# Kernel optimization log

Hardware: AMD Instinct MI355X
Metric: run time of the kernel (lower is better)

Reference implementation:

```python
import jax, jax.numpy as jnp
import numpy as np

B, N, D_MODEL, H, D_K, D_V = 2, 2048, 1024, 16, 64, 64


def setup_inputs() -> dict:
    key = jax.random.key(0)
    ks = jax.random.split(key, 8)
    queries = jax.random.normal(ks[0], (B, N, D_MODEL), dtype=jnp.float32)
    keys = jax.random.normal(ks[1], (B, N, D_MODEL), dtype=jnp.float32)
    values = jax.random.normal(ks[2], (B, N, D_MODEL), dtype=jnp.float32)
    # nn.Linear weights: (out_features, in_features); init.normal_(std=0.001) in the
    # original, but we use a larger scale for a numerically meaningful test.
    Wq = jax.random.normal(ks[3], (H * D_K, D_MODEL), dtype=jnp.float32) * 0.02
    Wk = jax.random.normal(ks[4], (H * D_K, D_MODEL), dtype=jnp.float32) * 0.02
    Wv = jax.random.normal(ks[5], (H * D_V, D_MODEL), dtype=jnp.float32) * 0.02
    Wo = jax.random.normal(ks[6], (D_MODEL, H * D_V), dtype=jnp.float32) * 0.02
    bo = jnp.zeros((D_MODEL,), dtype=jnp.float32)
    return {"queries": queries, "keys": keys, "values": values,
            "Wq": Wq, "Wk": Wk, "Wv": Wv, "Wo": Wo, "bo": bo}


def reference(queries, keys, values, Wq, Wk, Wv, Wo, bo):
    b, nq, _ = queries.shape
    nk = keys.shape[1]
    scale = 1.0 / np.sqrt(D_K).astype(np.float32)
    # projections: (b, n, h, d)
    q = (queries @ Wq.T).reshape(b, nq, H, D_K)
    k = (keys @ Wk.T).reshape(b, nk, H, D_K)
    v = (values @ Wv.T).reshape(b, nk, H, D_V)
    # scaled dot-product attention; seq_mask=None, attention_weights=None, dropout p=0
    att = jnp.einsum('bqhd,bkhd->bhqk', q, k) * scale  # (b, h, nq, nk)
    att = jax.nn.softmax(att, axis=-1)
    out = jnp.einsum('bhqk,bkhd->bqhd', att, v).reshape(b, nq, H * D_V)
    return queries + (out @ Wo.T + bo)
```

## Files before the change

### kernel.cpp

```cpp
#include <hip/hip_runtime.h>
#include <hip/hip_bf16.h>
#include <stdint.h>

#define BATCH  2
#define SEQ    2048
#define DMODEL 1024
#define NHEAD  16
#define DHEAD  64

typedef unsigned short u16;
typedef __attribute__((ext_vector_type(8))) short bf16x8;
typedef __attribute__((ext_vector_type(4))) float f32x4;

__device__ __forceinline__ u16 f2bf(float x) {
    union { float f; uint32_t u; } v; v.f = x;
    uint32_t r = v.u + 0x7fffu + ((v.u >> 16) & 1u);
    return (u16)(r >> 16);
}

__device__ __forceinline__ uint32_t pk2bf(float a, float b) {
    __hip_bfloat162 h = __float22bfloat162_rn(make_float2(a, b));
    return *(uint32_t*)&h;
}

__device__ __forceinline__ float exp2_raw(float x) {
    float r;
    asm("v_exp_f32 %0, %1" : "=v"(r) : "v"(x));
    return r;
}

__device__ __forceinline__ void gload_lds16(const void* g, void* l) {
    __builtin_amdgcn_global_load_lds(
        (const __attribute__((address_space(1))) uint32_t*)(uintptr_t)g,
        (__attribute__((address_space(3))) uint32_t*)(uintptr_t)l,
        16, 0, 0);
}

__device__ __forceinline__ f32x4 mfma16(bf16x8 a, bf16x8 b, f32x4 c) {
    return __builtin_amdgcn_mfma_f32_16x16x32_bf16(a, b, c, 0, 0, 0);
}

__global__ __launch_bounds__(256) void cvt7_kernel(
    const float* s0, const float* s1, const float* s2, const float* s3,
    const float* s4, const float* s5, const float* s6,
    u16* d0, u16* d1, u16* d2, u16* d3, u16* d4, u16* d5, u16* d6)
{
    const float* s; u16* d; size_t n;
    switch (blockIdx.y) {
        case 0: s = s0; d = d0; n = (size_t)BATCH * SEQ * DMODEL; break;
        case 1: s = s1; d = d1; n = (size_t)BATCH * SEQ * DMODEL; break;
        case 2: s = s2; d = d2; n = (size_t)BATCH * SEQ * DMODEL; break;
        case 3: s = s3; d = d3; n = (size_t)DMODEL * DMODEL; break;
        case 4: s = s4; d = d4; n = (size_t)DMODEL * DMODEL; break;
        case 5: s = s5; d = d5; n = (size_t)DMODEL * DMODEL; break;
        default: s = s6; d = d6; n = (size_t)DMODEL * DMODEL; break;
    }
    size_t i = ((size_t)blockIdx.x * 256 + threadIdx.x) * 8;
    if (i >= n) return;
    float4 a = *(const float4*)(s + i);
    float4 b = *(const float4*)(s + i + 4);
    union { uint4 v; u16 e[8]; } u;
    u.e[0] = f2bf(a.x); u.e[1] = f2bf(a.y); u.e[2] = f2bf(a.z); u.e[3] = f2bf(a.w);
    u.e[4] = f2bf(b.x); u.e[5] = f2bf(b.y); u.e[6] = f2bf(b.z); u.e[7] = f2bf(b.w);
    *(uint4*)(d + i) = u.v;
}

__device__ __forceinline__ void gemm_core_128(
    const u16* __restrict__ A, const u16* __restrict__ Bm, int K,
    int brow, int bcol, u16* As, u16* Bs, f32x4 (&acc)[4][4])
{
    const int tid  = threadIdx.x;
    const int lane = tid & 63;
    const int wr   = ((tid >> 6) >> 1) * 64;
    const int wc   = ((tid >> 6) & 1) * 64;
    const int srow = tid >> 2;
    const int scol = (tid & 3) * 8;
    const int fr   = lane & 15;
    const int fk   = (lane >> 4) * 8;

    for (int k0 = 0; k0 < K; k0 += 32) {
        gload_lds16(A  + (size_t)(brow + srow) * K + k0 + scol,       As + srow * 32 + scol);
        gload_lds16(A  + (size_t)(brow + 64 + srow) * K + k0 + scol,  As + (64 + srow) * 32 + scol);
        gload_lds16(Bm + (size_t)(bcol + srow) * K + k0 + scol,       Bs + srow * 32 + scol);
        gload_lds16(Bm + (size_t)(bcol + 64 + srow) * K + k0 + scol,  Bs + (64 + srow) * 32 + scol);
        __syncthreads();
        bf16x8 af[4], bfv[4];
        #pragma unroll
        for (int i = 0; i < 4; ++i) {
            af[i]  = *(const bf16x8*)(As + (wr + i * 16 + fr) * 32 + fk);
            bfv[i] = *(const bf16x8*)(Bs + (wc + i * 16 + fr) * 32 + fk);
        }
        #pragma unroll
        for (int am = 0; am < 4; ++am)
            #pragma unroll
            for (int bn = 0; bn < 4; ++bn)
                acc[am][bn] = mfma16(af[am], bfv[bn], acc[am][bn]);
        __syncthreads();
    }
}

__device__ __forceinline__ void gemm_core_64x128(
    const u16* __restrict__ A, const u16* __restrict__ Bm, int K,
    int brow, int bcol, u16* As, u16* Bs, f32x4 (&acc)[4][2])
{
    const int tid  = threadIdx.x;
    const int lane = tid & 63;
    const int wc   = (tid >> 6) * 32;
    const int srow = tid >> 2;
    const int scol = (tid & 3) * 8;
    const int fr   = lane & 15;
    const int fk   = (lane >> 4) * 8;

    for (int k0 = 0; k0 < K; k0 += 32) {
        gload_lds16(A  + (size_t)(brow + srow) * K + k0 + scol,       As + srow * 32 + scol);
        gload_lds16(Bm + (size_t)(bcol + srow) * K + k0 + scol,       Bs + srow * 32 + scol);
        gload_lds16(Bm + (size_t)(bcol + 64 + srow) * K + k0 + scol,  Bs + (64 + srow) * 32 + scol);
        __syncthreads();
        bf16x8 af[4], bfv[2];
        #pragma unroll
        for (int i = 0; i < 4; ++i)
            af[i]  = *(const bf16x8*)(As + (i * 16 + fr) * 32 + fk);
        #pragma unroll
        for (int i = 0; i < 2; ++i)
            bfv[i] = *(const bf16x8*)(Bs + (wc + i * 16 + fr) * 32 + fk);
        #pragma unroll
        for (int am = 0; am < 4; ++am)
            #pragma unroll
            for (int bn = 0; bn < 2; ++bn)
                acc[am][bn] = mfma16(af[am], bfv[bn], acc[am][bn]);
        __syncthreads();
    }
}

__global__ __launch_bounds__(256) void gemm_qkv_kernel(
    const u16* __restrict__ Xq, const u16* __restrict__ Xk, const u16* __restrict__ Xv,
    const u16* __restrict__ Wq, const u16* __restrict__ Wk, const u16* __restrict__ Wv,
    u16* __restrict__ Qo, u16* __restrict__ Ko, u16* __restrict__ Vt,
    int M, int Nn, int K)
{
    __shared__ u16 As[128 * 32];
    __shared__ u16 Bs[128 * 32];
    const int z = blockIdx.z;
    const u16* A  = (z == 0) ? Xq : (z == 1) ? Xk : Xv;
    const u16* Bm = (z == 0) ? Wq : (z == 1) ? Wk : Wv;
    const float scale = (z == 0) ? 0.18033688011112042f : 1.0f;

    const int lin  = blockIdx.y * gridDim.x + blockIdx.x;
    const int nlin = (lin & 7) * 32 + (lin >> 3);
    const int brow = (nlin >> 3) * 128;
    const int bcol = (nlin & 7) * 128;
    f32x4 acc[4][4];
    #pragma unroll
    for (int am = 0; am < 4; ++am)
        #pragma unroll
        for (int bn = 0; bn < 4; ++bn)
            acc[am][bn] = (f32x4){0.f, 0.f, 0.f, 0.f};

    gemm_core_128(A, Bm, K, brow, bcol, As, Bs, acc);

    const int lane = threadIdx.x & 63;
    const int wr = ((threadIdx.x >> 6) >> 1) * 64;
    const int wc = ((threadIdx.x >> 6) & 1) * 64;
    const int fr = lane & 15;
    const int fj4 = (lane >> 4) * 4;

    if (z == 2) {
        #pragma unroll
        for (int am = 0; am < 4; ++am)
            #pragma unroll
            for (int bn = 0; bn < 4; ++bn) {
                int row = brow + wr + am * 16 + fj4;
                int col = bcol + wc + bn * 16 + fr;
                int b   = row >> 11;
                int n   = row & 2047;
                int h   = col >> 6;
                int d   = col & 63;
                uint2 w;
                w.x = pk2bf(acc[am][bn][0], acc[am][bn][1]);
                w.y = pk2bf(acc[am][bn][2], acc[am][bn][3]);
                *(uint2*)(Vt + ((size_t)(b * 16 + h) * DHEAD + d) * SEQ + n) = w;
            }
    } else {
        u16* D = (z == 0) ? Qo : Ko;
        #pragma unroll
        for (int am = 0; am < 4; ++am)
            #pragma unroll
            for (int bn = 0; bn < 4; ++bn)
                #pragma unroll
                for (int j = 0; j < 4; ++j) {
                    int row = brow + wr + am * 16 + fj4 + j;
                    int col = bcol + wc + bn * 16 + fr;
                    D[(size_t)row * Nn + col] = f2bf(acc[am][bn][j] * scale);
                }
    }
}

__global__ __launch_bounds__(256, 2) void gemm_out_kernel(
    const u16* __restrict__ A, const u16* __restrict__ Bm,
    const float* __restrict__ bias, const float* __restrict__ resid,
    float* __restrict__ D, int M, int Nn, int K)
{
    __shared__ u16 As[64 * 32];
    __shared__ u16 Bs[128 * 32];

    const int lin  = blockIdx.y * gridDim.x + blockIdx.x;
    const int nlin = (lin & 7) * 64 + (lin >> 3);
    const int brow = (nlin >> 3) * 64;
    const int bcol = (nlin & 7) * 128;
    f32x4 acc[4][2];
    #pragma unroll
    for (int am = 0; am < 4; ++am)
        #pragma unroll
        for (int bn = 0; bn < 2; ++bn)
            acc[am][bn] = (f32x4){0.f, 0.f, 0.f, 0.f};

    gemm_core_64x128(A, Bm, K, brow, bcol, As, Bs, acc);

    const int lane = threadIdx.x & 63;
    const int wc = (threadIdx.x >> 6) * 32;
    const int fr = lane & 15;
    const int fj4 = (lane >> 4) * 4;
    #pragma unroll
    for (int am = 0; am < 4; ++am)
        #pragma unroll
        for (int bn = 0; bn < 2; ++bn)
            #pragma unroll
            for (int j = 0; j < 4; ++j) {
                int row = brow + am * 16 + fj4 + j;
                int col = bcol + wc + bn * 16 + fr;
                D[(size_t)row * Nn + col] = acc[am][bn][j] + bias[col] + resid[(size_t)row * Nn + col];
            }
}

__global__ __launch_bounds__(1024, 1) void attn_kernel(
    const u16* __restrict__ Qb, const u16* __restrict__ Kb, const u16* __restrict__ Vt,
    u16* __restrict__ AO)
{
    __shared__ u16 Ks[3][64 * 64];
    __shared__ u16 Vs[3][64 * 64];
    __shared__ u16 Ps[256 * 72];

    const int tid  = threadIdx.x;
    const int lane = tid & 63;
    const int wave = tid >> 6;

    const int lin  = blockIdx.x;
    const int nlin = (lin & 7) * 32 + (lin >> 3);
    const int qblk = nlin & 7;
    const int bh   = nlin >> 3;

    const size_t rowbase = (size_t)(bh >> 4) * SEQ;
    const int colbase = (bh & 15) * DHEAD;
    const int q0 = qblk * 256;
    const int fr  = lane & 15;
    const int g   = lane >> 4;
    const int fk  = g * 8;
    const int fj4 = g * 4;
    const int qw  = wave * 16;

    const u16* Kh = Kb + rowbase * DMODEL + colbase;
    const u16* Vh = Vt + (size_t)bh * DHEAD * SEQ;

    const int st  = tid & 511;
    const int sr  = st >> 3;
    const int sc  = st & 7;
    const int scs = (sc ^ (sr & 7)) << 3;
    const int sdst = sr * 64 + sc * 8;
    const bool stageK = (tid < 512);

    bf16x8 qf[2];
    #pragma unroll
    for (int kc = 0; kc < 2; ++kc)
        qf[kc] = *(const bf16x8*)(Qb + (rowbase + q0 + qw + fr) * DMODEL
                                     + colbase + kc * 32 + fk);

    f32x4 oacc[4];
    float lsum = 0.f;
    #pragma unroll
    for (int dn = 0; dn < 4; ++dn) oacc[dn] = (f32x4){0.f, 0.f, 0.f, 0.f};

    if (stageK) {
        gload_lds16(Kh + (size_t)sr * DMODEL + scs,        &Ks[0][sdst]);
        gload_lds16(Kh + (size_t)(64 + sr) * DMODEL + scs, &Ks[1][sdst]);
    } else {
        gload_lds16(Vh + (size_t)sr * SEQ + scs,           &Vs[0][sdst]);
        gload_lds16(Vh + (size_t)sr * SEQ + 64 + scs,      &Vs[1][sdst]);
    }

    const int NT = SEQ / 64;
    int cur = 0;
    for (int t = 0; t < NT; ++t) {
        if (t < NT - 1) {
            asm volatile("s_waitcnt vmcnt(1)" ::: "memory");
        } else {
            asm volatile("s_waitcnt vmcnt(0)" ::: "memory");
        }
        __builtin_amdgcn_s_barrier();
        __builtin_amdgcn_sched_barrier(0);

        if (t + 2 < NT) {
            int wbuf = cur + 2; if (wbuf >= 3) wbuf -= 3;
            const size_t kvn = (size_t)(t + 2) * 64;
            if (stageK) gload_lds16(Kh + (kvn + sr) * DMODEL + scs,    &Ks[wbuf][sdst]);
            else        gload_lds16(Vh + (size_t)sr * SEQ + kvn + scs, &Vs[wbuf][sdst]);
        }

        const u16* K0 = &Ks[cur][0];
        const u16* V0 = &Vs[cur][0];

        f32x4 sacc[4];
        #pragma unroll
        for (int bn = 0; bn < 4; ++bn) sacc[bn] = (f32x4){0.f, 0.f, 0.f, 0.f};
        __builtin_amdgcn_s_setprio(1);
        #pragma unroll
        for (int bn = 0; bn < 4; ++bn) {
            bf16x8 kf0 = *(const bf16x8*)(K0 + (bn * 16 + fr) * 64 + (((g)     ^ (fr & 7)) << 3));
            bf16x8 kf1 = *(const bf16x8*)(K0 + (bn * 16 + fr) * 64 + (((4 + g) ^ (fr & 7)) << 3));
            sacc[bn] = mfma16(kf0, qf[0], sacc[bn]);
            sacc[bn] = mfma16(kf1, qf[1], sacc[bn]);
        }
        __builtin_amdgcn_s_setprio(0);

        {
            float lacc = 0.f;
            #pragma unroll
            for (int bn = 0; bn < 4; ++bn) {
                float p0 = exp2_raw(sacc[bn][0]);
                float p1 = exp2_raw(sacc[bn][1]);
                float p2 = exp2_raw(sacc[bn][2]);
                float p3 = exp2_raw(sacc[bn][3]);
                uint2 w;
                w.x = pk2bf(p0, p1);
                w.y = pk2bf(p2, p3);
                *(uint2*)(Ps + (qw + fr) * 72 + bn * 16 + fj4) = w;
                lacc += (p0 + p1) + (p2 + p3);
            }
            lsum += lacc;
        }

        bf16x8 pf[2];
        #pragma unroll
        for (int kc = 0; kc < 2; ++kc)
            pf[kc] = *(const bf16x8*)(Ps + (qw + fr) * 72 + kc * 32 + fk);
        __builtin_amdgcn_s_setprio(1);
        #pragma unroll
        for (int dn = 0; dn < 4; ++dn) {
            bf16x8 vf0 = *(const bf16x8*)(V0 + (dn * 16 + fr) * 64 + (((g)     ^ (fr & 7)) << 3));
            bf16x8 vf1 = *(const bf16x8*)(V0 + (dn * 16 + fr) * 64 + (((4 + g) ^ (fr & 7)) << 3));
            oacc[dn] = mfma16(pf[0], vf0, oacc[dn]);
            oacc[dn] = mfma16(pf[1], vf1, oacc[dn]);
        }
        __builtin_amdgcn_s_setprio(0);

        cur = (cur == 2) ? 0 : cur + 1;
    }

    float invj[4];
    {
        float l = lsum;
        l += __shfl_xor(l, 16);
        l += __shfl_xor(l, 32);
        #pragma unroll
        for (int j = 0; j < 4; ++j) {
            float lj = __shfl(l, (lane & 48) | (fj4 + j));
            invj[j] = 1.f / lj;
        }
    }

    #pragma unroll
    for (int dn = 0; dn < 4; ++dn)
        #pragma unroll
        for (int j = 0; j < 4; ++j) {
            int row = q0 + qw + fj4 + j;
            AO[(rowbase + row) * DMODEL + colbase + dn * 16 + fr] =
                f2bf(oacc[dn][j] * invj[j]);
        }
}

extern "C" void kernel_launch(void* const* d_in, const int* in_sizes, int n_in,
                              void* d_out, int out_size, void* d_ws, size_t ws_size,
                              hipStream_t stream)
{
    const float* q_f  = (const float*)d_in[0];
    const float* k_f  = (const float*)d_in[1];
    const float* v_f  = (const float*)d_in[2];
    const float* Wq_f = (const float*)d_in[3];
    const float* Wk_f = (const float*)d_in[4];
    const float* Wv_f = (const float*)d_in[5];
    const float* Wo_f = (const float*)d_in[6];
    const float* bo_f = (const float*)d_in[7];

    char* ws = (char*)d_ws;
    const size_t ACT = (size_t)BATCH * SEQ * DMODEL * sizeof(u16);
    const size_t WSZ = (size_t)DMODEL * DMODEL * sizeof(u16);
    u16* Xq  = (u16*)(ws);
    u16* Xk  = (u16*)(ws + ACT);
    u16* Xv  = (u16*)(ws + 2 * ACT);
    u16* Wqb = (u16*)(ws + 3 * ACT);
    u16* Wkb = (u16*)(ws + 3 * ACT + WSZ);
    u16* Wvb = (u16*)(ws + 3 * ACT + 2 * WSZ);
    u16* Wob = (u16*)(ws + 3 * ACT + 3 * WSZ);
    u16* Qb  = (u16*)(ws + 3 * ACT + 4 * WSZ);
    u16* Kb  = (u16*)(ws + 4 * ACT + 4 * WSZ);
    u16* Vt  = (u16*)(ws + 5 * ACT + 4 * WSZ);
    u16* AO  = (u16*)(ws + 6 * ACT + 4 * WSZ);

    const int M = BATCH * SEQ;
    const int Nn = DMODEL;
    const int K = DMODEL;

    cvt7_kernel<<<dim3(2048, 7, 1), 256, 0, stream>>>(
        q_f, k_f, v_f, Wq_f, Wk_f, Wv_f, Wo_f,
        Xq, Xk, Xv, Wqb, Wkb, Wvb, Wob);

    gemm_qkv_kernel<<<dim3(Nn / 128, M / 128, 3), 256, 0, stream>>>(
        Xq, Xk, Xv, Wqb, Wkb, Wvb, Qb, Kb, Vt, M, Nn, K);

    attn_kernel<<<dim3(256, 1, 1), 1024, 0, stream>>>(Qb, Kb, Vt, AO);

    gemm_out_kernel<<<dim3(Nn / 128, M / 64, 1), 256, 0, stream>>>(
        AO, Wob, bo_f, q_f, (float*)d_out, M, Nn, K);
}
```

Before: 123.4 us.

## Fuse fp32-to-bf16 activation conversion into QKV GEMM A-tile loads

The standalone conversion pass over the three fp32 activation tensors is removed. The QKV GEMM now reads the fp32 activations directly, converts them to bf16 in registers and stores them into LDS, while the weights are still pre-converted by a smaller kernel. This avoids writing and re-reading roughly 24 MB of bf16 activation copies. In exchange the A loads now go through registers instead of the async global-to-LDS path, each tile re-reads fp32 data at twice the byte width, and every column tile repeats the conversion.

```diff
diff --git a/kernel.cpp b/kernel.cpp
--- a/kernel.cpp
+++ b/kernel.cpp
@@ -40,23 +40,18 @@
     return __builtin_amdgcn_mfma_f32_16x16x32_bf16(a, b, c, 0, 0, 0);
 }
 
-__global__ __launch_bounds__(256) void cvt7_kernel(
+__global__ __launch_bounds__(256) void cvt4_kernel(
     const float* s0, const float* s1, const float* s2, const float* s3,
-    const float* s4, const float* s5, const float* s6,
-    u16* d0, u16* d1, u16* d2, u16* d3, u16* d4, u16* d5, u16* d6)
-{
-    const float* s; u16* d; size_t n;
+    u16* d0, u16* d1, u16* d2, u16* d3)
+{
+    const float* s; u16* d;
     switch (blockIdx.y) {
-        case 0: s = s0; d = d0; n = (size_t)BATCH * SEQ * DMODEL; break;
-        case 1: s = s1; d = d1; n = (size_t)BATCH * SEQ * DMODEL; break;
-        case 2: s = s2; d = d2; n = (size_t)BATCH * SEQ * DMODEL; break;
-        case 3: s = s3; d = d3; n = (size_t)DMODEL * DMODEL; break;
-        case 4: s = s4; d = d4; n = (size_t)DMODEL * DMODEL; break;
-        case 5: s = s5; d = d5; n = (size_t)DMODEL * DMODEL; break;
-        default: s = s6; d = d6; n = (size_t)DMODEL * DMODEL; break;
+        case 0: s = s0; d = d0; break;
+        case 1: s = s1; d = d1; break;
+        case 2: s = s2; d = d2; break;
+        default: s = s3; d = d3; break;
     }
     size_t i = ((size_t)blockIdx.x * 256 + threadIdx.x) * 8;
-    if (i >= n) return;
     float4 a = *(const float4*)(s + i);
     float4 b = *(const float4*)(s + i + 4);
     union { uint4 v; u16 e[8]; } u;
@@ -65,8 +60,8 @@
     *(uint4*)(d + i) = u.v;
 }
 
-__device__ __forceinline__ void gemm_core_128(
-    const u16* __restrict__ A, const u16* __restrict__ Bm, int K,
+__device__ __forceinline__ void gemm_core_128_f32A(
+    const float* __restrict__ A, const u16* __restrict__ Bm, int K,
     int brow, int bcol, u16* As, u16* Bs, f32x4 (&acc)[4][4])
 {
     const int tid  = threadIdx.x;
@@ -79,8 +74,21 @@
     const int fk   = (lane >> 4) * 8;
 
     for (int k0 = 0; k0 < K; k0 += 32) {
-        gload_lds16(A  + (size_t)(brow + srow) * K + k0 + scol,       As + srow * 32 + scol);
-        gload_lds16(A  + (size_t)(brow + 64 + srow) * K + k0 + scol,  As + (64 + srow) * 32 + scol);
+        {
+            const float* s0 = A + (size_t)(brow + srow) * K + k0 + scol;
+            const float* s1 = A + (size_t)(brow + 64 + srow) * K + k0 + scol;
+            float4 a0 = *(const float4*)(s0);
+            float4 a1 = *(const float4*)(s0 + 4);
+            float4 b0 = *(const float4*)(s1);
+            float4 b1 = *(const float4*)(s1 + 4);
+            uint4 wA, wB;
+            wA.x = pk2bf(a0.x, a0.y); wA.y = pk2bf(a0.z, a0.w);
+            wA.z = pk2bf(a1.x, a1.y); wA.w = pk2bf(a1.z, a1.w);
+            wB.x = pk2bf(b0.x, b0.y); wB.y = pk2bf(b0.z, b0.w);
+            wB.z = pk2bf(b1.x, b1.y); wB.w = pk2bf(b1.z, b1.w);
+            *(uint4*)(As + srow * 32 + scol) = wA;
+            *(uint4*)(As + (64 + srow) * 32 + scol) = wB;
+        }
         gload_lds16(Bm + (size_t)(bcol + srow) * K + k0 + scol,       Bs + srow * 32 + scol);
         gload_lds16(Bm + (size_t)(bcol + 64 + srow) * K + k0 + scol,  Bs + (64 + srow) * 32 + scol);
         __syncthreads();
@@ -133,7 +141,7 @@
 }
 
 __global__ __launch_bounds__(256) void gemm_qkv_kernel(
-    const u16* __restrict__ Xq, const u16* __restrict__ Xk, const u16* __restrict__ Xv,
+    const float* __restrict__ Xq, const float* __restrict__ Xk, const float* __restrict__ Xv,
     const u16* __restrict__ Wq, const u16* __restrict__ Wk, const u16* __restrict__ Wv,
     u16* __restrict__ Qo, u16* __restrict__ Ko, u16* __restrict__ Vt,
     int M, int Nn, int K)
@@ -141,8 +149,8 @@
     __shared__ u16 As[128 * 32];
     __shared__ u16 Bs[128 * 32];
     const int z = blockIdx.z;
-    const u16* A  = (z == 0) ? Xq : (z == 1) ? Xk : Xv;
-    const u16* Bm = (z == 0) ? Wq : (z == 1) ? Wk : Wv;
+    const float* A = (z == 0) ? Xq : (z == 1) ? Xk : Xv;
+    const u16* Bm  = (z == 0) ? Wq : (z == 1) ? Wk : Wv;
     const float scale = (z == 0) ? 0.18033688011112042f : 1.0f;
 
     const int lin  = blockIdx.y * gridDim.x + blockIdx.x;
@@ -156,7 +164,7 @@
         for (int bn = 0; bn < 4; ++bn)
             acc[am][bn] = (f32x4){0.f, 0.f, 0.f, 0.f};
 
-    gemm_core_128(A, Bm, K, brow, bcol, As, Bs, acc);
+    gemm_core_128_f32A(A, Bm, K, brow, bcol, As, Bs, acc);
 
     const int lane = threadIdx.x & 63;
     const int wr = ((threadIdx.x >> 6) >> 1) * 64;
@@ -393,28 +401,24 @@
     char* ws = (char*)d_ws;
     const size_t ACT = (size_t)BATCH * SEQ * DMODEL * sizeof(u16);
     const size_t WSZ = (size_t)DMODEL * DMODEL * sizeof(u16);
-    u16* Xq  = (u16*)(ws);
-    u16* Xk  = (u16*)(ws + ACT);
-    u16* Xv  = (u16*)(ws + 2 * ACT);
-    u16* Wqb = (u16*)(ws + 3 * ACT);
-    u16* Wkb = (u16*)(ws + 3 * ACT + WSZ);
-    u16* Wvb = (u16*)(ws + 3 * ACT + 2 * WSZ);
-    u16* Wob = (u16*)(ws + 3 * ACT + 3 * WSZ);
-    u16* Qb  = (u16*)(ws + 3 * ACT + 4 * WSZ);
-    u16* Kb  = (u16*)(ws + 4 * ACT + 4 * WSZ);
-    u16* Vt  = (u16*)(ws + 5 * ACT + 4 * WSZ);
-    u16* AO  = (u16*)(ws + 6 * ACT + 4 * WSZ);
+    u16* Wqb = (u16*)(ws);
+    u16* Wkb = (u16*)(ws + WSZ);
+    u16* Wvb = (u16*)(ws + 2 * WSZ);
+    u16* Wob = (u16*)(ws + 3 * WSZ);
+    u16* Qb  = (u16*)(ws + 4 * WSZ);
+    u16* Kb  = (u16*)(ws + 4 * WSZ + ACT);
+    u16* Vt  = (u16*)(ws + 4 * WSZ + 2 * ACT);
+    u16* AO  = (u16*)(ws + 4 * WSZ + 3 * ACT);
 
     const int M = BATCH * SEQ;
     const int Nn = DMODEL;
     const int K = DMODEL;
 
-    cvt7_kernel<<<dim3(2048, 7, 1), 256, 0, stream>>>(
-        q_f, k_f, v_f, Wq_f, Wk_f, Wv_f, Wo_f,
-        Xq, Xk, Xv, Wqb, Wkb, Wvb, Wob);
+    cvt4_kernel<<<dim3(512, 4, 1), 256, 0, stream>>>(
+        Wq_f, Wk_f, Wv_f, Wo_f, Wqb, Wkb, Wvb, Wob);
 
     gemm_qkv_kernel<<<dim3(Nn / 128, M / 128, 3), 256, 0, stream>>>(
-        Xq, Xk, Xv, Wqb, Wkb, Wvb, Qb, Kb, Vt, M, Nn, K);
+        q_f, k_f, v_f, Wqb, Wkb, Wvb, Qb, Kb, Vt, M, Nn, K);
 
     attn_kernel<<<dim3(256, 1, 1), 1024, 0, stream>>>(Qb, Kb, Vt, AO);
 
```

After: 120.3 us. 1.03x faster.
